# Kernel tuning notes

Measured on AMD Instinct MI355X. Metric: run time of the kernel, lower is better.

Reference implementation:

```python
import jax, jax.numpy as jnp
import numpy as np
import math

B, T, C, H = 4, 2048, 1024, 16
D = C // H  # head dim = 64


def setup_inputs() -> dict:
    key = jax.random.key(0)
    k1, k2, k3, k4, k5 = jax.random.split(key, 5)
    scale = 1.0 / math.sqrt(C)
    return {
        "x": jax.random.normal(k1, (B, T, C), dtype=jnp.float32),
        "w_attn": jax.random.normal(k2, (C, 3 * C), dtype=jnp.float32) * scale,
        "b_attn": jax.random.normal(k3, (3 * C,), dtype=jnp.float32) * 0.02,
        "w_proj": jax.random.normal(k4, (C, C), dtype=jnp.float32) * scale,
        "b_proj": jax.random.normal(k5, (C,), dtype=jnp.float32) * 0.02,
    }


def reference(x, w_attn, b_attn, w_proj, b_proj):
    Bx, Tx, Cx = x.shape
    qkv = x @ w_attn + b_attn                      # [B,T,3C]
    q, k, v = jnp.split(qkv, 3, axis=-1)           # each [B,T,C]
    # reshape to [B,H,T,D]
    q = q.reshape(Bx, Tx, H, D).transpose(0, 2, 1, 3)
    k = k.reshape(Bx, Tx, H, D).transpose(0, 2, 1, 3)
    v = v.reshape(Bx, Tx, H, D).transpose(0, 2, 1, 3)
    att = jnp.einsum("bhqd,bhkd->bhqk", q, k) * (1.0 / math.sqrt(D))
    causal = jnp.tril(jnp.ones((Tx, Tx), dtype=bool))
    att = jnp.where(causal, att, -jnp.inf)
    att = jax.nn.softmax(att, axis=-1)
    y = jnp.einsum("bhqk,bhkd->bhqd", att, v)      # [B,H,T,D]
    y = y.transpose(0, 2, 1, 3).reshape(Bx, Tx, Cx)
    return y @ w_proj + b_proj
```

## Files before the change

kernel.cpp:

```cpp
#include <hip/hip_runtime.h>
#include <hip/hip_bf16.h>
#include <stdint.h>

typedef unsigned short u16;
typedef unsigned int u32;
typedef __attribute__((ext_vector_type(8))) __bf16 bf16x8;
typedef __attribute__((ext_vector_type(4))) float f32x4;
typedef __attribute__((ext_vector_type(16))) float f32x16;

#define B_ 4
#define T_ 2048
#define C_ 1024
#define H_ 16
#define D_ 64

__device__ __forceinline__ u16 f2bf(float f) {
  union { float f; u32 u; } v; v.f = f;
  u32 r = (v.u + 0x7fffu + ((v.u >> 16) & 1u)) >> 16;
  return (u16)r;
}

__device__ __forceinline__ float fexp2(float x) {
  float r;
  asm("v_exp_f32 %0, %1\n\ts_nop 0" : "=v"(r) : "v"(x));
  return r;
}

__device__ __forceinline__ u32 cvtpk(float lo, float hi2) {
  u32 r;
  asm("v_cvt_pk_bf16_f32 %0, %1, %2" : "=v"(r) : "v"(lo), "v"(hi2));
  return r;
}

__device__ __forceinline__ void gll16(const void* g, void* l) {
  __builtin_amdgcn_global_load_lds((const __attribute__((address_space(1))) void*)g,
                                   (__attribute__((address_space(3))) void*)l, 16, 0, 0);
}

__global__ void k_prep(const float* __restrict__ x, u16* __restrict__ xb,
                       const float* __restrict__ wa, u16* __restrict__ waT,
                       const float* __restrict__ wp, u16* __restrict__ wpT) {
  __shared__ float tile[32][33];
  const int bid = blockIdx.x;
  const int tx = threadIdx.x, ty = threadIdx.y;
  if (bid < 2048) {
    const int tid = bid * 256 + ty * 32 + tx;
    const int n4 = (B_ * T_ * C_) / 4;
    for (int i = tid; i < n4; i += 2048 * 256) {
      float4 v = ((const float4*)x)[i];
      ushort4 o;
      o.x = f2bf(v.x); o.y = f2bf(v.y); o.z = f2bf(v.z); o.w = f2bf(v.w);
      ((ushort4*)xb)[i] = o;
    }
    return;
  }
  const float* src; u16* dst; int N, b2;
  if (bid < 5120) { b2 = bid - 2048; src = wa; dst = waT; N = 3 * C_; }
  else            { b2 = bid - 5120; src = wp; dst = wpT; N = C_; }
  const int K = C_;
  const int k0 = (b2 & 31) * 32, n0 = (b2 >> 5) * 32;
#pragma unroll
  for (int r = 0; r < 4; ++r) {
    int k = ty + r * 8;
    tile[k][tx] = src[(size_t)(k0 + k) * N + n0 + tx];
  }
  __syncthreads();
#pragma unroll
  for (int r = 0; r < 4; ++r) {
    int n = ty + r * 8;
    dst[(size_t)(n0 + n) * K + k0 + tx] = f2bf(tile[tx][n]);
  }
}

template <int MODE>
__global__ __launch_bounds__(256) void k_gemm(
    const u16* __restrict__ A, const u16* __restrict__ BT, const float* __restrict__ bias,
    float* __restrict__ outF, u16* __restrict__ qb, u16* __restrict__ kb, u16* __restrict__ vbT,
    int M, int N, int K) {
  __shared__ u16 al[3][128 * 32];
  __shared__ u16 bl[3][128 * 32];
  const int lane = threadIdx.x & 63, wid = threadIdx.x >> 6;
  const int nbx = N >> 7;
  const int cpx = ((M >> 7) * nbx) >> 3;
  const int wg = blockIdx.x;
  const int lid = (wg & 7) * cpx + (wg >> 3);
  const int brow = (lid / nbx) * 128, bcol = (lid % nbx) * 128;
  const int wr = (wid >> 1) * 64, wc = (wid & 1) * 64;
  const int lr = lane & 15, lg = lane >> 4, lk = lg * 8;
  f32x4 acc[4][4] = {};

  auto stage = [&](u16* ad, u16* bd, int t2) {
    const int kt = t2 * 32;
#pragma unroll
    for (int it = 0; it < 2; ++it) {
      int cbase = (wid * 2 + it) * 64;
      int c = cbase + lane;
      int row = c >> 2, col = (c & 3) * 8;
      gll16(A + (size_t)(brow + row) * K + kt + col, ad + cbase * 8);
      gll16(BT + (size_t)(bcol + row) * K + kt + col, bd + cbase * 8);
    }
  };

  const int nt = K / 32;
  stage(al[0], bl[0], 0);
  stage(al[1], bl[1], 1);

  for (int t = 0; t < nt; ++t) {
    if (t == nt - 1) { asm volatile("s_waitcnt vmcnt(0)" ::: "memory"); }
    else             { asm volatile("s_waitcnt vmcnt(4)" ::: "memory"); }
    __builtin_amdgcn_sched_barrier(0);
    __builtin_amdgcn_s_barrier();
    __builtin_amdgcn_sched_barrier(0);

    const int nxt = t + 2;
    if (nxt < nt) {
      const int ib = nxt % 3;
      stage(al[ib], bl[ib], nxt);
    }

    const u16* ab = al[t % 3];
    const u16* bb = bl[t % 3];
    bf16x8 af[4], bfr[4];
#pragma unroll
    for (int m = 0; m < 4; ++m) af[m] = *(const bf16x8*)&ab[(wr + m * 16 + lr) * 32 + lk];
#pragma unroll
    for (int n = 0; n < 4; ++n) bfr[n] = *(const bf16x8*)&bb[(wc + n * 16 + lr) * 32 + lk];

    __builtin_amdgcn_s_setprio(1);
#pragma unroll
    for (int m = 0; m < 4; ++m)
#pragma unroll
      for (int n = 0; n < 4; ++n)
        acc[m][n] = __builtin_amdgcn_mfma_f32_16x16x32_bf16(af[m], bfr[n], acc[m][n], 0, 0, 0);
    __builtin_amdgcn_s_setprio(0);
  }

#pragma unroll
  for (int m = 0; m < 4; ++m) {
    int row = brow + wr + m * 16 + lg * 4;
#pragma unroll
    for (int n = 0; n < 4; ++n) {
      int col = bcol + wc + n * 16 + lr;
      float bs = bias[col];
      if (MODE == 0) {
#pragma unroll
        for (int r = 0; r < 4; ++r)
          outF[(size_t)(row + r) * N + col] = acc[m][n][r] + bs;
      } else {
        int sec = col >> 10, cc = col & 1023;
        int h = cc >> 6, dd = cc & 63;
        int b = row >> 11, t = row & 2047;
        size_t bh = (size_t)(b * H_ + h);
        if (sec < 2) {
          u16* dst = (sec == 0 ? qb : kb) + (bh * T_ + t) * D_ + dd;
#pragma unroll
          for (int r = 0; r < 4; ++r) dst[(size_t)r * D_] = f2bf(acc[m][n][r] + bs);
        } else {
          ushort4 pk;
          pk.x = f2bf(acc[m][n][0] + bs);
          pk.y = f2bf(acc[m][n][1] + bs);
          pk.z = f2bf(acc[m][n][2] + bs);
          pk.w = f2bf(acc[m][n][3] + bs);
          *(ushort4*)&vbT[(bh * D_ + dd) * T_ + t] = pk;
        }
      }
    }
  }
}

__global__ __launch_bounds__(256) void k_attn(
    const u16* __restrict__ qb, const u16* __restrict__ kb,
    const u16* __restrict__ vbT, u16* __restrict__ attb) {
  __shared__ u16 kl0[64 * 64], kl1[64 * 64];
  __shared__ u16 vl0[64 * 64], vl1[64 * 64];
  const int lane = threadIdx.x & 63, wid = threadIdx.x >> 6;
  const int w = blockIdx.x;
  const int lid = (w & 7) * 64 + (w >> 3);
  const int bh = lid >> 3, qpair = lid & 7;
  const int b = bh >> 4, h = bh & 15;
  const int l31 = lane & 31, hi = lane >> 5;
  const int sw3 = l31 & 7;

  const float SC = 0.18033688f;

  const u16* kbase = kb + (size_t)bh * T_ * D_;
  const u16* vbase = vbT + (size_t)bh * D_ * T_;

  auto stage = [&](u16* kd, u16* vd, int kt) {
    const int k0 = kt * 64;
#pragma unroll
    for (int it = 0; it < 2; ++it) {
      int cbase = (wid * 2 + it) * 64;
      int c = cbase + lane;
      int cs = (c & ~7) | ((c ^ (c >> 3)) & 7);
      gll16(kbase + (size_t)k0 * D_ + (size_t)cs * 8, kd + cbase * 8);
      int vrow = cs >> 3, vcol = (cs & 7) * 8;
      gll16(vbase + (size_t)vrow * T_ + k0 + vcol, vd + cbase * 8);
    }
  };

  auto pack = [&](const f32x16& s, bf16x8* out) {
#pragma unroll
    for (int cc = 0; cc < 2; ++cc) {
      const int rb = cc * 8;
      u32 a  = cvtpk(s[rb + 0], s[rb + 1]);
      u32 c  = cvtpk(s[rb + 2], s[rb + 3]);
      u32 bb = cvtpk(s[rb + 4], s[rb + 5]);
      u32 d  = cvtpk(s[rb + 6], s[rb + 7]);
      u32 as = __shfl_xor(a, 32, 64), cs = __shfl_xor(c, 32, 64);
      u32 bs = __shfl_xor(bb, 32, 64), ds = __shfl_xor(d, 32, 64);
      union { u32 u[4]; bf16x8 v; } t;
      t.u[0] = hi ? bs : a;
      t.u[1] = hi ? ds : c;
      t.u[2] = hi ? bb : as;
      t.u[3] = hi ? d : cs;
      out[cc] = t.v;
    }
  };

#pragma unroll 1
  for (int pass = 0; pass < 2; ++pass) {
    const int qbk = pass ? (15 - qpair) : qpair;
    const int qw = qbk * 128 + wid * 32;

    const u16* qrow = qb + ((size_t)bh * T_ + qw + l31) * D_ + hi * 8;
    bf16x8 qf[4];
#pragma unroll
    for (int j = 0; j < 4; ++j) qf[j] = *(const bf16x8*)(qrow + j * 16);

    float lsum = 0.f;
    f32x16 o0 = {}, o1 = {};

    const int nt = 2 * qbk + 2;
    const int lastkt = (qw + 31) >> 6;

    auto compute = [&](const u16* kl, const u16* vl, int kt) {
      const int k0 = kt * 64;
      f32x16 s0 = {}, s1 = {};
      __builtin_amdgcn_s_setprio(1);
#pragma unroll
      for (int j = 0; j < 4; ++j) {
        const int ch = ((2 * j + hi) ^ sw3) << 3;
        const bf16x8 kf0 = *(const bf16x8*)&kl[l31 * 64 + ch];
        const bf16x8 kf1 = *(const bf16x8*)&kl[(l31 + 32) * 64 + ch];
        s0 = __builtin_amdgcn_mfma_f32_32x32x16_bf16(kf0, qf[j], s0, 0, 0, 0);
        s1 = __builtin_amdgcn_mfma_f32_32x32x16_bf16(kf1, qf[j], s1, 0, 0, 0);
      }
      __builtin_amdgcn_s_setprio(0);

      if (kt == lastkt) {
        const int q = qw + l31;
#pragma unroll
        for (int r = 0; r < 16; ++r) {
          const int kv = k0 + (r & 3) + 8 * (r >> 2) + 4 * hi;
          if (kv > q) s0[r] = -3e38f;
          if (kv + 32 > q) s1[r] = -3e38f;
        }
      }

#pragma unroll
      for (int r = 0; r < 16; ++r) s0[r] = fexp2(s0[r] * SC);
      float t0[8];
#pragma unroll
      for (int r = 0; r < 8; ++r) t0[r] = s0[r] + s0[r + 8];
#pragma unroll
      for (int w2 = 4; w2 >= 1; w2 >>= 1)
#pragma unroll
        for (int r = 0; r < 4; ++r)
          if (r < w2) t0[r] += t0[r + w2];

      bf16x8 pb0[2];
      pack(s0, pb0);
      __builtin_amdgcn_s_setprio(1);
#pragma unroll
      for (int c = 0; c < 2; ++c) {
        const int ch = ((2 * c + hi) ^ sw3) << 3;
        const bf16x8 vf0 = *(const bf16x8*)&vl[l31 * 64 + ch];
        const bf16x8 vf1 = *(const bf16x8*)&vl[(l31 + 32) * 64 + ch];
        o0 = __builtin_amdgcn_mfma_f32_32x32x16_bf16(vf0, pb0[c], o0, 0, 0, 0);
        o1 = __builtin_amdgcn_mfma_f32_32x32x16_bf16(vf1, pb0[c], o1, 0, 0, 0);
      }
      __builtin_amdgcn_s_setprio(0);

#pragma unroll
      for (int r = 0; r < 16; ++r) s1[r] = fexp2(s1[r] * SC);
      float t1[8];
#pragma unroll
      for (int r = 0; r < 8; ++r) t1[r] = s1[r] + s1[r + 8];
#pragma unroll
      for (int w2 = 4; w2 >= 1; w2 >>= 1)
#pragma unroll
        for (int r = 0; r < 4; ++r)
          if (r < w2) t1[r] += t1[r + w2];

      bf16x8 pb1[2];
      pack(s1, pb1);
      __builtin_amdgcn_s_setprio(1);
#pragma unroll
      for (int c = 2; c < 4; ++c) {
        const int ch = ((2 * c + hi) ^ sw3) << 3;
        const bf16x8 vf0 = *(const bf16x8*)&vl[l31 * 64 + ch];
        const bf16x8 vf1 = *(const bf16x8*)&vl[(l31 + 32) * 64 + ch];
        o0 = __builtin_amdgcn_mfma_f32_32x32x16_bf16(vf0, pb1[c - 2], o0, 0, 0, 0);
        o1 = __builtin_amdgcn_mfma_f32_32x32x16_bf16(vf1, pb1[c - 2], o1, 0, 0, 0);
      }
      __builtin_amdgcn_s_setprio(0);

      float ps = t0[0] + t1[0];
      ps += __shfl_xor(ps, 32, 64);
      lsum += ps;
    };

    stage(kl0, vl0, 0);
    __syncthreads();
    int kt = 0;
    while (true) {
      if (kt + 1 < nt) stage(kl1, vl1, kt + 1);
      if (kt <= lastkt) compute(kl0, vl0, kt);
      __syncthreads();
      if (++kt >= nt) break;
      if (kt + 1 < nt) stage(kl0, vl0, kt + 1);
      if (kt <= lastkt) compute(kl1, vl1, kt);
      __syncthreads();
      if (++kt >= nt) break;
    }

    const float inv = 1.0f / lsum;
    u16* orow = attb + ((size_t)b * T_ + qw + l31) * C_ + h * D_;
#pragma unroll
    for (int rg = 0; rg < 4; ++rg) {
      ushort4 w0, w1;
      w0.x = f2bf(o0[rg * 4 + 0] * inv); w0.y = f2bf(o0[rg * 4 + 1] * inv);
      w0.z = f2bf(o0[rg * 4 + 2] * inv); w0.w = f2bf(o0[rg * 4 + 3] * inv);
      w1.x = f2bf(o1[rg * 4 + 0] * inv); w1.y = f2bf(o1[rg * 4 + 1] * inv);
      w1.z = f2bf(o1[rg * 4 + 2] * inv); w1.w = f2bf(o1[rg * 4 + 3] * inv);
      const int d0 = rg * 8 + hi * 4;
      *(ushort4*)(orow + d0) = w0;
      *(ushort4*)(orow + d0 + 32) = w1;
    }
  }
}

extern "C" void kernel_launch(void* const* d_in, const int* in_sizes, int n_in,
                              void* d_out, int out_size, void* d_ws, size_t ws_size,
                              hipStream_t stream) {
  const float* x = (const float*)d_in[0];
  const float* w_attn = (const float*)d_in[1];
  const float* b_attn = (const float*)d_in[2];
  const float* w_proj = (const float*)d_in[3];
  const float* b_proj = (const float*)d_in[4];
  float* out = (float*)d_out;

  char* ws = (char*)d_ws;
  const size_t MB = 1024 * 1024;
  u16* xb   = (u16*)(ws);
  u16* attb = xb;
  u16* waT  = (u16*)(ws + 16 * MB);
  u16* wpT  = (u16*)(ws + 22 * MB);
  u16* qb   = (u16*)(ws + 24 * MB);
  u16* kb   = (u16*)(ws + 40 * MB);
  u16* vbT  = (u16*)(ws + 56 * MB);

  k_prep<<<6144, dim3(32, 8), 0, stream>>>(x, xb, w_attn, waT, w_proj, wpT);

  k_gemm<1><<<(8192 / 128) * (3 * C_ / 128), 256, 0, stream>>>(
      xb, waT, b_attn, nullptr, qb, kb, vbT, B_ * T_, 3 * C_, C_);

  k_attn<<<512, 256, 0, stream>>>(qb, kb, vbT, attb);

  k_gemm<0><<<(8192 / 128) * (C_ / 128), 256, 0, stream>>>(
      attb, wpT, b_proj, out, nullptr, nullptr, nullptr, B_ * T_, C_, C_);
}
```

Measured before the change: 169.0 us.

## Triple-buffer K/V tiles in attention with a single barrier per iteration

Replaces the double-buffered K/V shared-memory staging with a three-deep ring buffer that prefetches two tiles ahead. It waits with explicit vmcnt counts and one raw s_barrier per tile instead of two __syncthreads, so global loads overlap more with MFMA work. The cross-lane shuffle for the softmax row sum also moves out of the per-tile loop into a single reduction at the end. The cost is 50% more LDS per block, which may lower occupancy, and correctness now relies on the hand-set vmcnt value matching the number of loads issued by stage.

```diff
diff --git a/kernel.cpp b/kernel.cpp
--- a/kernel.cpp
+++ b/kernel.cpp
@@ -171,8 +171,8 @@
 __global__ __launch_bounds__(256) void k_attn(
     const u16* __restrict__ qb, const u16* __restrict__ kb,
     const u16* __restrict__ vbT, u16* __restrict__ attb) {
-  __shared__ u16 kl0[64 * 64], kl1[64 * 64];
-  __shared__ u16 vl0[64 * 64], vl1[64 * 64];
+  __shared__ u16 kl[3][64 * 64];
+  __shared__ u16 vl[3][64 * 64];
   const int lane = threadIdx.x & 63, wid = threadIdx.x >> 6;
   const int w = blockIdx.x;
   const int lid = (w & 7) * 64 + (w >> 3);
@@ -234,15 +234,15 @@
     const int nt = 2 * qbk + 2;
     const int lastkt = (qw + 31) >> 6;
 
-    auto compute = [&](const u16* kl, const u16* vl, int kt) {
+    auto compute = [&](const u16* klp, const u16* vlp, int kt) {
       const int k0 = kt * 64;
       f32x16 s0 = {}, s1 = {};
       __builtin_amdgcn_s_setprio(1);
 #pragma unroll
       for (int j = 0; j < 4; ++j) {
         const int ch = ((2 * j + hi) ^ sw3) << 3;
-        const bf16x8 kf0 = *(const bf16x8*)&kl[l31 * 64 + ch];
-        const bf16x8 kf1 = *(const bf16x8*)&kl[(l31 + 32) * 64 + ch];
+        const bf16x8 kf0 = *(const bf16x8*)&klp[l31 * 64 + ch];
+        const bf16x8 kf1 = *(const bf16x8*)&klp[(l31 + 32) * 64 + ch];
         s0 = __builtin_amdgcn_mfma_f32_32x32x16_bf16(kf0, qf[j], s0, 0, 0, 0);
         s1 = __builtin_amdgcn_mfma_f32_32x32x16_bf16(kf1, qf[j], s1, 0, 0, 0);
       }
@@ -275,8 +275,8 @@
 #pragma unroll
       for (int c = 0; c < 2; ++c) {
         const int ch = ((2 * c + hi) ^ sw3) << 3;
-        const bf16x8 vf0 = *(const bf16x8*)&vl[l31 * 64 + ch];
-        const bf16x8 vf1 = *(const bf16x8*)&vl[(l31 + 32) * 64 + ch];
+        const bf16x8 vf0 = *(const bf16x8*)&vlp[l31 * 64 + ch];
+        const bf16x8 vf1 = *(const bf16x8*)&vlp[(l31 + 32) * 64 + ch];
         o0 = __builtin_amdgcn_mfma_f32_32x32x16_bf16(vf0, pb0[c], o0, 0, 0, 0);
         o1 = __builtin_amdgcn_mfma_f32_32x32x16_bf16(vf1, pb0[c], o1, 0, 0, 0);
       }
@@ -299,33 +299,35 @@
 #pragma unroll
       for (int c = 2; c < 4; ++c) {
         const int ch = ((2 * c + hi) ^ sw3) << 3;
-        const bf16x8 vf0 = *(const bf16x8*)&vl[l31 * 64 + ch];
-        const bf16x8 vf1 = *(const bf16x8*)&vl[(l31 + 32) * 64 + ch];
+        const bf16x8 vf0 = *(const bf16x8*)&vlp[l31 * 64 + ch];
+        const bf16x8 vf1 = *(const bf16x8*)&vlp[(l31 + 32) * 64 + ch];
         o0 = __builtin_amdgcn_mfma_f32_32x32x16_bf16(vf0, pb1[c - 2], o0, 0, 0, 0);
         o1 = __builtin_amdgcn_mfma_f32_32x32x16_bf16(vf1, pb1[c - 2], o1, 0, 0, 0);
       }
       __builtin_amdgcn_s_setprio(0);
 
-      float ps = t0[0] + t1[0];
-      ps += __shfl_xor(ps, 32, 64);
-      lsum += ps;
+      lsum += t0[0] + t1[0];
     };
 
-    stage(kl0, vl0, 0);
-    __syncthreads();
-    int kt = 0;
-    while (true) {
-      if (kt + 1 < nt) stage(kl1, vl1, kt + 1);
-      if (kt <= lastkt) compute(kl0, vl0, kt);
-      __syncthreads();
-      if (++kt >= nt) break;
-      if (kt + 1 < nt) stage(kl0, vl0, kt + 1);
-      if (kt <= lastkt) compute(kl1, vl1, kt);
-      __syncthreads();
-      if (++kt >= nt) break;
-    }
-
-    const float inv = 1.0f / lsum;
+    stage(kl[0], vl[0], 0);
+    stage(kl[1], vl[1], 1);
+    for (int t = 0; t < nt; ++t) {
+      if (t == nt - 1) { asm volatile("s_waitcnt vmcnt(0)" ::: "memory"); }
+      else             { asm volatile("s_waitcnt vmcnt(4)" ::: "memory"); }
+      __builtin_amdgcn_sched_barrier(0);
+      __builtin_amdgcn_s_barrier();
+      __builtin_amdgcn_sched_barrier(0);
+
+      const int nxt = t + 2;
+      if (nxt < nt) {
+        const int ib = nxt % 3;
+        stage(kl[ib], vl[ib], nxt);
+      }
+      if (t <= lastkt) compute(kl[t % 3], vl[t % 3], t);
+    }
+
+    const float ls = lsum + __shfl_xor(lsum, 32, 64);
+    const float inv = 1.0f / ls;
     u16* orow = attb + ((size_t)b * T_ + qw + l31) * C_ + h * D_;
 #pragma unroll
     for (int rg = 0; rg < 4; ++rg) {
@@ -338,6 +340,8 @@
       *(ushort4*)(orow + d0) = w0;
       *(ushort4*)(orow + d0 + 32) = w1;
     }
+
+    __syncthreads();
   }
 }
 
```

Result: no change. 171.4 us (+1.4%).
